# Performance work log

Hardware: AMD Instinct MI355X
Metric: run time of the kernel (lower is better)

Reference implementation:

```python
import jax, jax.numpy as jnp
import numpy as np

B, N_ROIS, C, H, W = 4, 180, 512, 48, 48
STRIDE = 4
EPS = 1e-5


def _pool_one(feat, roi):
    # feat: [C,H,W], roi: [4] float (y1,x1,y2,x2) in image coords
    r = roi / STRIDE
    r0 = jnp.trunc(r[0]).astype(jnp.int32)
    r1 = jnp.trunc(r[1]).astype(jnp.int32)
    r2 = jnp.ceil(r[2]).astype(jnp.int32)
    r3 = jnp.ceil(r[3]).astype(jnp.int32)
    h_size = r2 - r0 + 1
    w_size = r3 - r1 + 1
    idx2 = jnp.arange(2)
    # AdaptiveMaxPool2d region boundaries: [floor(i*s/2), ceil((i+1)*s/2))
    sh = (idx2 * h_size) // 2
    eh = ((idx2 + 1) * h_size + 1) // 2
    sw = (idx2 * w_size) // 2
    ew = ((idx2 + 1) * w_size + 1) // 2
    hh = jnp.arange(H)[None, :]
    ww = jnp.arange(W)[None, :]
    mask_h = (hh >= (r0 + sh)[:, None]) & (hh < (r0 + eh)[:, None])  # [2,H]
    mask_w = (ww >= (r1 + sw)[:, None]) & (ww < (r1 + ew)[:, None])  # [2,W]
    neg = jnp.finfo(feat.dtype).min
    # max over W within each col region -> [2(oj), C, H]
    mw = jnp.where(mask_w[:, None, None, :], feat[None], neg).max(axis=-1)
    # max over H within each row region -> [2(oi), 2(oj), C]
    p = jnp.where(mask_h[:, None, None, :], mw[None], neg).max(axis=-1)
    # torch layout: [C, oi, oj] then flatten row-major
    return jnp.transpose(p, (2, 0, 1)).reshape(-1)  # [C*4]


def _roi_pool(features, rois):
    # features: [B,C,H,W], rois: [B,N,4] -> [B,N,C*4]
    def per_roi(roi_b):  # roi_b: [B,4]
        return jax.vmap(_pool_one)(features, roi_b)  # [B, C*4]
    out = jax.lax.map(per_roi, jnp.swapaxes(rois, 0, 1))  # [N,B,C*4]
    return jnp.swapaxes(out, 0, 1)


def _bn(x, gamma, beta):
    # training-mode BatchNorm1d over [B, N_ROIS(channels), F]: stats over (B,F)
    mean = x.mean(axis=(0, 2), keepdims=True)
    var = ((x - mean) ** 2).mean(axis=(0, 2), keepdims=True)
    return (x - mean) * jax.lax.rsqrt(var + EPS) * gamma[None, :, None] + beta[None, :, None]


def setup_inputs() -> dict:
    key = jax.random.key(0)
    k1, k2, k3, k4, k5 = jax.random.split(key, 5)
    features = jax.random.normal(k1, (B, C, H, W), dtype=jnp.float32)
    max_coord = (H - 1) * STRIDE
    y = jnp.sort(jax.random.uniform(k2, (B, N_ROIS, 2), minval=0.0, maxval=max_coord), axis=-1)
    x = jnp.sort(jax.random.uniform(k3, (B, N_ROIS, 2), minval=0.0, maxval=max_coord), axis=-1)
    rois = jnp.stack([y[..., 0], x[..., 0], y[..., 1], x[..., 1]], axis=-1)  # [B,N,4]
    F_in = C * 4
    W1 = jax.random.normal(k4, (64, F_in), dtype=jnp.float32) * 0.02
    bl1 = jnp.zeros((64,), dtype=jnp.float32)
    gamma1 = jnp.ones((N_ROIS,), dtype=jnp.float32)
    beta1 = jnp.zeros((N_ROIS,), dtype=jnp.float32)
    gamma2 = jnp.ones((N_ROIS,), dtype=jnp.float32)
    beta2 = jnp.zeros((N_ROIS,), dtype=jnp.float32)
    return {"features": features, "rois": rois, "gamma1": gamma1, "beta1": beta1,
            "W1": W1, "bl1": bl1, "gamma2": gamma2, "beta2": beta2}


def reference(features, rois, gamma1, beta1, W1, bl1, gamma2, beta2):
    pooled = _roi_pool(features, rois)            # [B, 180, 2048]
    x = jax.nn.relu(pooled)
    x = _bn(x, gamma1, beta1)
    y = jnp.einsum('bnf,of->bno', x, W1) + bl1    # [B, 180, 64]
    y = _bn(y, gamma2, beta2)
    return y
```

## Files before the change

kernel.cpp:

```cpp
#include <hip/hip_runtime.h>
#include <hip/hip_bf16.h>
#include <cfloat>
#include <math.h>

#define BB 4
#define NR 180
#define CC 512
#define HH 48
#define WW 48
#define FF (CC*4)
#define OO 64
#define EPSV 1e-5f
#define TW_LEVEL ((size_t)BB*HH*WW*CC)


typedef unsigned short us2 __attribute__((ext_vector_type(2)));

__device__ __forceinline__ unsigned pmax(unsigned a, unsigned b) {
    return __builtin_bit_cast(unsigned, __builtin_elementwise_max(
        __builtin_bit_cast(us2, a), __builtin_bit_cast(us2, b)));
}
__device__ __forceinline__ uint4 pmax4(uint4 a, uint4 b) {
    return make_uint4(pmax(a.x,b.x), pmax(a.y,b.y), pmax(a.z,b.z), pmax(a.w,b.w));
}
__device__ __forceinline__ unsigned mapb(float f) {
    unsigned fu = __float_as_uint(f);
    unsigned u = fu >> 16;
    return (fu >> 31) ? (~u & 0xFFFFu) : (u | 0x8000u);
}
__device__ __forceinline__ void unmap2(unsigned m, float& lo, float& hi) {
    unsigned t = ((~m) >> 15) & 0x00010001u;
    unsigned u = m ^ (0x80008000u ^ (t * 0x7FFFu));
    lo = __uint_as_float(u << 16);
    hi = __uint_as_float(u & 0xffff0000u);
}

__global__ __launch_bounds__(256) void k_prep(const float* __restrict__ feat,
                                              const float* __restrict__ W1,
                                              ushort* __restrict__ featB,
                                              float* __restrict__ W1T4) {
    __shared__ float tile[32][33];
    int t = threadIdx.x;
    int z = blockIdx.z;

    if (z < 4) {
        const int S = HH * WW;
        int b  = z;
        int s0 = blockIdx.x * 32;
        int c0 = blockIdx.y * 32;
        const float* src = feat + (size_t)b * CC * S;
        ushort* dst = featB + (size_t)b * S * CC;

        int cl = t >> 3;
        int sx = (t & 7) << 2;
        float4 v = *(const float4*)(src + (size_t)(c0 + cl) * S + s0 + sx);
        tile[cl][sx] = v.x; tile[cl][sx+1] = v.y; tile[cl][sx+2] = v.z; tile[cl][sx+3] = v.w;
        __syncthreads();

        int sl = t >> 3;
        int c4 = (t & 7) << 2;
        unsigned u0 = mapb(tile[c4][sl])   | (mapb(tile[c4+1][sl]) << 16);
        unsigned u1 = mapb(tile[c4+2][sl]) | (mapb(tile[c4+3][sl]) << 16);
        *(uint2*)(dst + (size_t)(s0 + sl) * CC + c0 + c4) = make_uint2(u0, u1);
    } else {
        if (blockIdx.x >= 8) return;
        int kt = blockIdx.y * 8 + blockIdx.x;
        int k0 = (kt >> 1) * 32, o0 = (kt & 1) * 32;
        int tx = t & 31, ty = t >> 5;
        #pragma unroll
        for (int k = 0; k < 4; k++) {
            int row = ty + k * 8;
            tile[row][tx] = W1[(size_t)(o0 + row) * FF + (k0 + tx)];
        }
        __syncthreads();
        #pragma unroll
        for (int k = 0; k < 4; k++) {
            int row = ty + k * 8;
            int kk = k0 + row;
            int o  = o0 + tx;
            W1T4[(size_t)(kk >> 2) * 256 + o * 4 + (kk & 3)] = tile[tx][row];
        }
    }
}

__global__ __launch_bounds__(256) void k_tab(const ushort* __restrict__ featB,
                                             ushort* __restrict__ Tw) {
    __shared__ uint4 A[WW][64];
    int by = blockIdx.x;
    int b = by / HH, y = by % HH;
    int t = threadIdx.x;
    const uint4* src = (const uint4*)(featB + (size_t)((b * HH + y) * WW) * CC);

    #pragma unroll
    for (int i = 0; i < 12; i++) {
        int it = t + i * 256;
        A[it >> 6][it & 63] = src[it];
    }
    __syncthreads();

    for (int k = 1; k <= 4; k++) {
        int h = 1 << (k - 1);
        uint4* dst = (uint4*)(Tw + ((size_t)(k - 1) * BB * HH + b * HH + y) * (size_t)(WW * CC));
        uint4 v[12];
        #pragma unroll
        for (int i = 0; i < 12; i++) {
            int it = t + i * 256;
            int x = it >> 6, c = it & 63;
            v[i] = pmax4(A[x][c], A[min(x + h, WW - 1)][c]);
        }
        __syncthreads();
        #pragma unroll
        for (int i = 0; i < 12; i++) {
            int it = t + i * 256;
            A[it >> 6][it & 63] = v[i];
            dst[it] = v[i];
        }
        __syncthreads();
    }
}

__global__ __launch_bounds__(1024) void k_pg(const ushort* __restrict__ featB,
                                             const ushort* __restrict__ Tw,
                                             const float* __restrict__ rois,
                                             const float* __restrict__ W1T4,
                                             const float* __restrict__ bl1,
                                             const float* __restrict__ g1,
                                             const float* __restrict__ b1,
                                             const float* __restrict__ g2,
                                             const float* __restrict__ b2,
                                             float* __restrict__ out) {
    __shared__ unsigned lu[BB][4][16][65];
    __shared__ float xs[BB][FF];
    __shared__ float pd[16][BB][OO];
    __shared__ float pw[16][OO];
    __shared__ float part_s[16], part_q[16];
    __shared__ float sm2[4], sq2[4];

    int n = blockIdx.x;
    int tid = threadIdx.x;
    int b  = tid >> 8;
    int g  = (tid >> 6) & 3;
    int c  = tid & 63;

    const float* roi = rois + ((size_t)b * NR + n) * 4;
    int r0 = (int)(roi[0] * 0.25f);
    int r1 = (int)(roi[1] * 0.25f);
    int r2 = (int)ceilf(roi[2] * 0.25f);
    int r3 = (int)ceilf(roi[3] * 0.25f);
    int hs  = r2 - r0 + 1;
    int wsz = r3 - r1 + 1;
    int eh0 = (hs + 1) >> 1, sh1 = hs >> 1;
    int ew0 = (wsz + 1) >> 1, sw1 = wsz >> 1;

    int len0 = ew0;
    int k0 = 31 - __clz(len0);
    int x0a = r1, x0b = r1 + len0 - (1 << k0);
    int len1 = wsz - sw1;
    int k1 = 31 - __clz(len1);
    int x1a = r1 + sw1, x1b = r1 + wsz - (1 << k1);

    const ushort* base0 = (k0 == 0) ? featB : (Tw + (size_t)(k0 - 1) * TW_LEVEL);
    const ushort* base1 = (k1 == 0) ? featB : (Tw + (size_t)(k1 - 1) * TW_LEVEL);

    const uint4 Z = make_uint4(0,0,0,0);
    uint4 q00 = Z, q01 = Z, q10 = Z, q11 = Z;
    for (int L = g; L < hs; L += 4) {
        size_t rowoff = (size_t)((b * HH + r0 + L) * WW) * CC;
        const uint4* p0 = (const uint4*)(base0 + rowoff) + c;
        const uint4* p1 = (const uint4*)(base1 + rowoff) + c;
        uint4 cm0 = pmax4(p0[(size_t)64 * x0a], p0[(size_t)64 * x0b]);
        uint4 cm1 = pmax4(p1[(size_t)64 * x1a], p1[(size_t)64 * x1b]);
        if (L <  eh0) { q00 = pmax4(q00, cm0); q01 = pmax4(q01, cm1); }
        if (L >= sh1) { q10 = pmax4(q10, cm0); q11 = pmax4(q11, cm1); }
    }

    {
        unsigned* L0 = &lu[b][g][0][c];
        unsigned a, p2;
        a = q00.x; p2 = q01.x;
        L0[ 0*65] = (a & 0xFFFFu) | (p2 << 16);
        L0[ 2*65] = (a >> 16)     | (p2 & 0xFFFF0000u);
        a = q10.x; p2 = q11.x;
        L0[ 1*65] = (a & 0xFFFFu) | (p2 << 16);
        L0[ 3*65] = (a >> 16)     | (p2 & 0xFFFF0000u);
        a = q00.y; p2 = q01.y;
        L0[ 4*65] = (a & 0xFFFFu) | (p2 << 16);
        L0[ 6*65] = (a >> 16)     | (p2 & 0xFFFF0000u);
        a = q10.y; p2 = q11.y;
        L0[ 5*65] = (a & 0xFFFFu) | (p2 << 16);
        L0[ 7*65] = (a >> 16)     | (p2 & 0xFFFF0000u);
        a = q00.z; p2 = q01.z;
        L0[ 8*65] = (a & 0xFFFFu) | (p2 << 16);
        L0[10*65] = (a >> 16)     | (p2 & 0xFFFF0000u);
        a = q10.z; p2 = q11.z;
        L0[ 9*65] = (a & 0xFFFFu) | (p2 << 16);
        L0[11*65] = (a >> 16)     | (p2 & 0xFFFF0000u);
        a = q00.w; p2 = q01.w;
        L0[12*65] = (a & 0xFFFFu) | (p2 << 16);
        L0[14*65] = (a >> 16)     | (p2 & 0xFFFF0000u);
        a = q10.w; p2 = q11.w;
        L0[13*65] = (a & 0xFFFFu) | (p2 << 16);
        L0[15*65] = (a >> 16)     | (p2 & 0xFFFF0000u);
    }
    __syncthreads();

    float s_acc = 0.f, q_acc = 0.f;
    int s  = tid & 255;
    int bb = tid >> 8;
    #pragma unroll
    for (int p = 0; p < 2; p++) {
        int fb = (p << 10) + (s << 2);
        int cc = fb >> 5;
        int j0 = (fb >> 1) & 15;
        unsigned m0 = pmax(pmax(lu[bb][0][j0  ][cc], lu[bb][1][j0  ][cc]),
                           pmax(lu[bb][2][j0  ][cc], lu[bb][3][j0  ][cc]));
        unsigned m1 = pmax(pmax(lu[bb][0][j0+1][cc], lu[bb][1][j0+1][cc]),
                           pmax(lu[bb][2][j0+1][cc], lu[bb][3][j0+1][cc]));
        m0 = pmax(m0, 0x80008000u);
        m1 = pmax(m1, 0x80008000u);
        float v0, v1, v2, v3;
        unmap2(m0, v0, v1);
        unmap2(m1, v2, v3);
        *(float4*)&xs[bb][fb] = make_float4(v0, v1, v2, v3);
        s_acc += v0 + v1 + v2 + v3;
        q_acc += v0*v0 + v1*v1 + v2*v2 + v3*v3;
    }
    for (int off = 32; off; off >>= 1) {
        s_acc += __shfl_down(s_acc, off);
        q_acc += __shfl_down(q_acc, off);
    }
    if ((tid & 63) == 0) { part_s[tid >> 6] = s_acc; part_q[tid >> 6] = q_acc; }
    __syncthreads();
    float ts = 0.f, tq = 0.f;
    #pragma unroll
    for (int i = 0; i < 16; i++) { ts += part_s[i]; tq += part_q[i]; }
    const float inv1 = 1.f / (float)(BB * FF);
    float mean = ts * inv1;
    float var  = tq * inv1 - mean * mean;
    float a1n  = g1[n] * rsqrtf(var + EPSV);
    float c1n  = b1[n] - mean * a1n;

    int sc = tid >> 6;
    int o  = tid & 63;
    int k4a = sc << 5;
    float a0 = 0.f, a1 = 0.f, a2 = 0.f, a3 = 0.f, wsum = 0.f;
    #pragma unroll 4
    for (int k4 = k4a; k4 < k4a + 32; k4++) {
        float4 w4 = *(const float4*)(W1T4 + (size_t)k4 * 256 + o * 4);
        float4 x0 = *(const float4*)&xs[0][k4 << 2];
        float4 x1 = *(const float4*)&xs[1][k4 << 2];
        float4 x2 = *(const float4*)&xs[2][k4 << 2];
        float4 x3 = *(const float4*)&xs[3][k4 << 2];
        wsum += w4.x + w4.y + w4.z + w4.w;
        a0 += w4.x*x0.x + w4.y*x0.y + w4.z*x0.z + w4.w*x0.w;
        a1 += w4.x*x1.x + w4.y*x1.y + w4.z*x1.z + w4.w*x1.w;
        a2 += w4.x*x2.x + w4.y*x2.y + w4.z*x2.z + w4.w*x2.w;
        a3 += w4.x*x3.x + w4.y*x3.y + w4.z*x3.z + w4.w*x3.w;
    }
    pd[sc][0][o] = a0; pd[sc][1][o] = a1; pd[sc][2][o] = a2; pd[sc][3][o] = a3;
    pw[sc][o] = wsum;
    __syncthreads();

    float y = 0.f;
    int bo = tid >> 6;
    if (tid < 256) {
        float dot = 0.f, wsm = 0.f;
        #pragma unroll
        for (int ss = 0; ss < 16; ss++) { dot += pd[ss][bo][o]; wsm += pw[ss][o]; }
        y = a1n * dot + c1n * wsm + bl1[o];
        float rs = y, rq = y * y;
        for (int off = 32; off; off >>= 1) {
            rs += __shfl_down(rs, off);
            rq += __shfl_down(rq, off);
        }
        if (o == 0) { sm2[bo] = rs; sq2[bo] = rq; }
    }
    __syncthreads();
    if (tid < 256) {
        float sm  = sm2[0] + sm2[1] + sm2[2] + sm2[3];
        float sqm = sq2[0] + sq2[1] + sq2[2] + sq2[3];
        const float inv2 = 1.f / 256.f;
        float mean2 = sm * inv2;
        float var2  = sqm * inv2 - mean2 * mean2;
        float r2s = rsqrtf(var2 + EPSV);
        out[((size_t)bo * NR + n) * OO + o] = (y - mean2) * r2s * g2[n] + b2[n];
    }
}

extern "C" void kernel_launch(void* const* d_in, const int* in_sizes, int n_in,
                              void* d_out, int out_size, void* d_ws, size_t ws_size,
                              hipStream_t stream) {
    const float* feat = (const float*)d_in[0];
    const float* rois = (const float*)d_in[1];
    const float* g1   = (const float*)d_in[2];
    const float* b1   = (const float*)d_in[3];
    const float* W1   = (const float*)d_in[4];
    const float* bl1  = (const float*)d_in[5];
    const float* g2   = (const float*)d_in[6];
    const float* b2   = (const float*)d_in[7];
    float* out = (float*)d_out;

    ushort* featB = (ushort*)d_ws;
    float*  W1T4  = (float*)(featB + (size_t)BB*HH*WW*CC);
    ushort* Tw    = (ushort*)(W1T4 + (size_t)OO*FF);

    k_prep<<<dim3(72, 16, 5), 256, 0, stream>>>(feat, W1, featB, W1T4);
    k_tab<<<dim3(BB * HH), 256, 0, stream>>>(featB, Tw);
    k_pg<<<dim3(NR), 1024, 0, stream>>>(featB, Tw, rois, W1T4, bl1, g1, b1, g2, b2, out);
}
```

Baseline: 108.0 us.

## Trim sparse-table levels to two and store pooled activations as packed bf16

The width sparse table now stores only the 4- and 8-wide levels instead of four levels, which cuts table-building writes. The pooling kernel then covers each column region with two or three loads from a single level instead of two power-of-two windows from per-region levels. The pooled activations are kept in shared memory as packed bf16 pairs rather than fp32, which halves shared-memory footprint and read traffic in the GEMV; the values are unpacked with shifts. The cost is an extra load for long regions and extra unpacking ALU work in the dot-product loop.

```diff
diff --git a/kernel.cpp b/kernel.cpp
--- a/kernel.cpp
+++ b/kernel.cpp
@@ -28,12 +28,15 @@
     unsigned u = fu >> 16;
     return (fu >> 31) ? (~u & 0xFFFFu) : (u | 0x8000u);
 }
-__device__ __forceinline__ void unmap2(unsigned m, float& lo, float& hi) {
+__device__ __forceinline__ unsigned unmap2u(unsigned m, float& lo, float& hi) {
     unsigned t = ((~m) >> 15) & 0x00010001u;
     unsigned u = m ^ (0x80008000u ^ (t * 0x7FFFu));
     lo = __uint_as_float(u << 16);
     hi = __uint_as_float(u & 0xffff0000u);
-}
+    return u;
+}
+#define BFLO(u) __uint_as_float((u) << 16)
+#define BFHI(u) __uint_as_float((u) & 0xffff0000u)
 
 __global__ __launch_bounds__(256) void k_prep(const float* __restrict__ feat,
                                               const float* __restrict__ W1,
@@ -98,9 +101,8 @@
     }
     __syncthreads();
 
-    for (int k = 1; k <= 4; k++) {
+    for (int k = 1; k <= 3; k++) {
         int h = 1 << (k - 1);
-        uint4* dst = (uint4*)(Tw + ((size_t)(k - 1) * BB * HH + b * HH + y) * (size_t)(WW * CC));
         uint4 v[12];
         #pragma unroll
         for (int i = 0; i < 12; i++) {
@@ -109,11 +111,20 @@
             v[i] = pmax4(A[x][c], A[min(x + h, WW - 1)][c]);
         }
         __syncthreads();
-        #pragma unroll
-        for (int i = 0; i < 12; i++) {
-            int it = t + i * 256;
-            A[it >> 6][it & 63] = v[i];
-            dst[it] = v[i];
+        if (k >= 2) {
+            uint4* dst = (uint4*)(Tw + ((size_t)(k - 2) * BB * HH + b * HH + y) * (size_t)(WW * CC));
+            #pragma unroll
+            for (int i = 0; i < 12; i++) {
+                int it = t + i * 256;
+                A[it >> 6][it & 63] = v[i];
+                dst[it] = v[i];
+            }
+        } else {
+            #pragma unroll
+            for (int i = 0; i < 12; i++) {
+                int it = t + i * 256;
+                A[it >> 6][it & 63] = v[i];
+            }
         }
         __syncthreads();
     }
@@ -130,7 +141,7 @@
                                              const float* __restrict__ b2,
                                              float* __restrict__ out) {
     __shared__ unsigned lu[BB][4][16][65];
-    __shared__ float xs[BB][FF];
+    __shared__ unsigned xsb[BB][FF/2];
     __shared__ float pd[16][BB][OO];
     __shared__ float pw[16][OO];
     __shared__ float part_s[16], part_q[16];
@@ -150,26 +161,28 @@
     int hs  = r2 - r0 + 1;
     int wsz = r3 - r1 + 1;
     int eh0 = (hs + 1) >> 1, sh1 = hs >> 1;
-    int ew0 = (wsz + 1) >> 1, sw1 = wsz >> 1;
-
-    int len0 = ew0;
-    int k0 = 31 - __clz(len0);
-    int x0a = r1, x0b = r1 + len0 - (1 << k0);
-    int len1 = wsz - sw1;
-    int k1 = 31 - __clz(len1);
-    int x1a = r1 + sw1, x1b = r1 + wsz - (1 << k1);
-
-    const ushort* base0 = (k0 == 0) ? featB : (Tw + (size_t)(k0 - 1) * TW_LEVEL);
-    const ushort* base1 = (k1 == 0) ? featB : (Tw + (size_t)(k1 - 1) * TW_LEVEL);
+    int sw1 = wsz >> 1;
+
+    int len = (wsz + 1) >> 1;
+    int ks  = (len >= 8) ? 3 : ((len >= 4) ? 2 : 0);
+    int w   = 1 << ks;
+    bool n3 = (len > 2 * w);
+    int xboff = (len >> 1) - (w >> 1);
+    int x0a = r1,        x0c = r1 + len - w,  x0b = r1 + xboff;
+    int x1a = r1 + sw1,  x1c = r1 + wsz - w,  x1b = r1 + sw1 + xboff;
+    const ushort* base = (ks == 0) ? featB : (Tw + (size_t)(ks - 2) * TW_LEVEL);
 
     const uint4 Z = make_uint4(0,0,0,0);
     uint4 q00 = Z, q01 = Z, q10 = Z, q11 = Z;
     for (int L = g; L < hs; L += 4) {
         size_t rowoff = (size_t)((b * HH + r0 + L) * WW) * CC;
-        const uint4* p0 = (const uint4*)(base0 + rowoff) + c;
-        const uint4* p1 = (const uint4*)(base1 + rowoff) + c;
-        uint4 cm0 = pmax4(p0[(size_t)64 * x0a], p0[(size_t)64 * x0b]);
-        uint4 cm1 = pmax4(p1[(size_t)64 * x1a], p1[(size_t)64 * x1b]);
+        const uint4* p = (const uint4*)(base + rowoff) + c;
+        uint4 cm0 = pmax4(p[(size_t)64 * x0a], p[(size_t)64 * x0c]);
+        uint4 cm1 = pmax4(p[(size_t)64 * x1a], p[(size_t)64 * x1c]);
+        if (n3) {
+            cm0 = pmax4(cm0, p[(size_t)64 * x0b]);
+            cm1 = pmax4(cm1, p[(size_t)64 * x1b]);
+        }
         if (L <  eh0) { q00 = pmax4(q00, cm0); q01 = pmax4(q01, cm1); }
         if (L >= sh1) { q10 = pmax4(q10, cm0); q11 = pmax4(q11, cm1); }
     }
@@ -219,9 +232,9 @@
         m0 = pmax(m0, 0x80008000u);
         m1 = pmax(m1, 0x80008000u);
         float v0, v1, v2, v3;
-        unmap2(m0, v0, v1);
-        unmap2(m1, v2, v3);
-        *(float4*)&xs[bb][fb] = make_float4(v0, v1, v2, v3);
+        unsigned u0 = unmap2u(m0, v0, v1);
+        unsigned u1 = unmap2u(m1, v2, v3);
+        *(uint2*)&xsb[bb][fb >> 1] = make_uint2(u0, u1);
         s_acc += v0 + v1 + v2 + v3;
         q_acc += v0*v0 + v1*v1 + v2*v2 + v3*v3;
     }
@@ -242,20 +255,26 @@
 
     int sc = tid >> 6;
     int o  = tid & 63;
-    int k4a = sc << 5;
     float a0 = 0.f, a1 = 0.f, a2 = 0.f, a3 = 0.f, wsum = 0.f;
     #pragma unroll 4
-    for (int k4 = k4a; k4 < k4a + 32; k4++) {
-        float4 w4 = *(const float4*)(W1T4 + (size_t)k4 * 256 + o * 4);
-        float4 x0 = *(const float4*)&xs[0][k4 << 2];
-        float4 x1 = *(const float4*)&xs[1][k4 << 2];
-        float4 x2 = *(const float4*)&xs[2][k4 << 2];
-        float4 x3 = *(const float4*)&xs[3][k4 << 2];
-        wsum += w4.x + w4.y + w4.z + w4.w;
-        a0 += w4.x*x0.x + w4.y*x0.y + w4.z*x0.z + w4.w*x0.w;
-        a1 += w4.x*x1.x + w4.y*x1.y + w4.z*x1.z + w4.w*x1.w;
-        a2 += w4.x*x2.x + w4.y*x2.y + w4.z*x2.z + w4.w*x2.w;
-        a3 += w4.x*x3.x + w4.y*x3.y + w4.z*x3.z + w4.w*x3.w;
+    for (int it = 0; it < 16; it++) {
+        int k4 = (sc << 5) + (it << 1);
+        float4 wa = *(const float4*)(W1T4 + (size_t)k4 * 256 + o * 4);
+        float4 wb = *(const float4*)(W1T4 + (size_t)(k4 + 1) * 256 + o * 4);
+        int pi = (sc << 6) + (it << 2);
+        uint4 v0p = *(const uint4*)&xsb[0][pi];
+        uint4 v1p = *(const uint4*)&xsb[1][pi];
+        uint4 v2p = *(const uint4*)&xsb[2][pi];
+        uint4 v3p = *(const uint4*)&xsb[3][pi];
+        wsum += wa.x + wa.y + wa.z + wa.w + wb.x + wb.y + wb.z + wb.w;
+        a0 += wa.x*BFLO(v0p.x) + wa.y*BFHI(v0p.x) + wa.z*BFLO(v0p.y) + wa.w*BFHI(v0p.y)
+            + wb.x*BFLO(v0p.z) + wb.y*BFHI(v0p.z) + wb.z*BFLO(v0p.w) + wb.w*BFHI(v0p.w);
+        a1 += wa.x*BFLO(v1p.x) + wa.y*BFHI(v1p.x) + wa.z*BFLO(v1p.y) + wa.w*BFHI(v1p.y)
+            + wb.x*BFLO(v1p.z) + wb.y*BFHI(v1p.z) + wb.z*BFLO(v1p.w) + wb.w*BFHI(v1p.w);
+        a2 += wa.x*BFLO(v2p.x) + wa.y*BFHI(v2p.x) + wa.z*BFLO(v2p.y) + wa.w*BFHI(v2p.y)
+            + wb.x*BFLO(v2p.z) + wb.y*BFHI(v2p.z) + wb.z*BFLO(v2p.w) + wb.w*BFHI(v2p.w);
+        a3 += wa.x*BFLO(v3p.x) + wa.y*BFHI(v3p.x) + wa.z*BFLO(v3p.y) + wa.w*BFHI(v3p.y)
+            + wb.x*BFLO(v3p.z) + wb.y*BFHI(v3p.z) + wb.z*BFLO(v3p.w) + wb.w*BFHI(v3p.w);
     }
     pd[sc][0][o] = a0; pd[sc][1][o] = a1; pd[sc][2][o] = a2; pd[sc][3][o] = a3;
     pw[sc][o] = wsum;
```

Result: slower. 111.8 us (+3.5%).

## Shrink sparse-table levels to widths 4 and 8, with a third probe when needed

Applied to the files above, without the earlier changes.

The table-building kernel now writes only the width-4 and width-8 max levels instead of four levels (widths 2 to 16), which cuts global writes and table memory. The pooling kernel picks one level for both column regions, since they have nearly equal length. It covers each span with two or three overlapping window reads, adding a middle probe when the span exceeds twice the window. This trades less table traffic and a shared base pointer for one extra load per row in some ROIs.

```diff
diff --git a/kernel.cpp b/kernel.cpp
--- a/kernel.cpp
+++ b/kernel.cpp
@@ -98,9 +98,8 @@
     }
     __syncthreads();
 
-    for (int k = 1; k <= 4; k++) {
+    for (int k = 1; k <= 3; k++) {
         int h = 1 << (k - 1);
-        uint4* dst = (uint4*)(Tw + ((size_t)(k - 1) * BB * HH + b * HH + y) * (size_t)(WW * CC));
         uint4 v[12];
         #pragma unroll
         for (int i = 0; i < 12; i++) {
@@ -109,11 +108,20 @@
             v[i] = pmax4(A[x][c], A[min(x + h, WW - 1)][c]);
         }
         __syncthreads();
-        #pragma unroll
-        for (int i = 0; i < 12; i++) {
-            int it = t + i * 256;
-            A[it >> 6][it & 63] = v[i];
-            dst[it] = v[i];
+        if (k >= 2) {
+            uint4* dst = (uint4*)(Tw + ((size_t)(k - 2) * BB * HH + b * HH + y) * (size_t)(WW * CC));
+            #pragma unroll
+            for (int i = 0; i < 12; i++) {
+                int it = t + i * 256;
+                A[it >> 6][it & 63] = v[i];
+                dst[it] = v[i];
+            }
+        } else {
+            #pragma unroll
+            for (int i = 0; i < 12; i++) {
+                int it = t + i * 256;
+                A[it >> 6][it & 63] = v[i];
+            }
         }
         __syncthreads();
     }
@@ -150,26 +158,28 @@
     int hs  = r2 - r0 + 1;
     int wsz = r3 - r1 + 1;
     int eh0 = (hs + 1) >> 1, sh1 = hs >> 1;
-    int ew0 = (wsz + 1) >> 1, sw1 = wsz >> 1;
-
-    int len0 = ew0;
-    int k0 = 31 - __clz(len0);
-    int x0a = r1, x0b = r1 + len0 - (1 << k0);
-    int len1 = wsz - sw1;
-    int k1 = 31 - __clz(len1);
-    int x1a = r1 + sw1, x1b = r1 + wsz - (1 << k1);
-
-    const ushort* base0 = (k0 == 0) ? featB : (Tw + (size_t)(k0 - 1) * TW_LEVEL);
-    const ushort* base1 = (k1 == 0) ? featB : (Tw + (size_t)(k1 - 1) * TW_LEVEL);
+    int sw1 = wsz >> 1;
+
+    int len = (wsz + 1) >> 1;
+    int ks  = (len >= 8) ? 3 : ((len >= 4) ? 2 : 0);
+    int w   = 1 << ks;
+    bool n3 = (len > 2 * w);
+    int xboff = (len >> 1) - (w >> 1);
+    int x0a = r1,        x0c = r1 + len - w,  x0b = r1 + xboff;
+    int x1a = r1 + sw1,  x1c = r1 + wsz - w,  x1b = r1 + sw1 + xboff;
+    const ushort* base = (ks == 0) ? featB : (Tw + (size_t)(ks - 2) * TW_LEVEL);
 
     const uint4 Z = make_uint4(0,0,0,0);
     uint4 q00 = Z, q01 = Z, q10 = Z, q11 = Z;
     for (int L = g; L < hs; L += 4) {
         size_t rowoff = (size_t)((b * HH + r0 + L) * WW) * CC;
-        const uint4* p0 = (const uint4*)(base0 + rowoff) + c;
-        const uint4* p1 = (const uint4*)(base1 + rowoff) + c;
-        uint4 cm0 = pmax4(p0[(size_t)64 * x0a], p0[(size_t)64 * x0b]);
-        uint4 cm1 = pmax4(p1[(size_t)64 * x1a], p1[(size_t)64 * x1b]);
+        const uint4* p = (const uint4*)(base + rowoff) + c;
+        uint4 cm0 = pmax4(p[(size_t)64 * x0a], p[(size_t)64 * x0c]);
+        uint4 cm1 = pmax4(p[(size_t)64 * x1a], p[(size_t)64 * x1c]);
+        if (n3) {
+            cm0 = pmax4(cm0, p[(size_t)64 * x0b]);
+            cm1 = pmax4(cm1, p[(size_t)64 * x1b]);
+        }
         if (L <  eh0) { q00 = pmax4(q00, cm0); q01 = pmax4(q01, cm1); }
         if (L >= sh1) { q10 = pmax4(q10, cm0); q11 = pmax4(q11, cm1); }
     }
```

Measured after the change: 110.4 us. 1.02x slower.
